# Performance work log

Measured on AMD Instinct MI355X. Metric: run time of the kernel, lower is better.

The kernel has to match this reference:

```python
import jax, jax.numpy as jnp
import numpy as np

EMB = 1024
NH = 16
HD = EMB // NH
FF = 4 * EMB
B, T = 2, 2048
LN_EPS = 1e-5


def setup_inputs() -> dict:
    key = jax.random.key(0)
    ks = jax.random.split(key, 16)
    s = 0.02
    return {
        "x": jax.random.normal(ks[0], (B, T, EMB), jnp.float32),
        "wq": jax.random.normal(ks[1], (EMB, EMB), jnp.float32) * s,
        "bq": jnp.zeros((EMB,), jnp.float32),
        "wk": jax.random.normal(ks[2], (EMB, EMB), jnp.float32) * s,
        "bk": jnp.zeros((EMB,), jnp.float32),
        "wv": jax.random.normal(ks[3], (EMB, EMB), jnp.float32) * s,
        "bv": jnp.zeros((EMB,), jnp.float32),
        "wo": jax.random.normal(ks[4], (EMB, EMB), jnp.float32) * s,
        "bo": jnp.zeros((EMB,), jnp.float32),
        "w1": jax.random.normal(ks[5], (EMB, FF), jnp.float32) * s,
        "b1": jnp.zeros((FF,), jnp.float32),
        "w2": jax.random.normal(ks[6], (FF, EMB), jnp.float32) * s,
        "b2": jnp.zeros((EMB,), jnp.float32),
        "ln1_g": jnp.ones((EMB,), jnp.float32),
        "ln1_b": jnp.zeros((EMB,), jnp.float32),
        "ln2_g": jnp.ones((EMB,), jnp.float32),
        "ln2_b": jnp.zeros((EMB,), jnp.float32),
        "alpha_attn": jnp.float32(0.5),
        "alpha_ff": jnp.float32(0.5),
    }


def _layernorm(x, g, b):
    mu = jnp.mean(x, axis=-1, keepdims=True)
    var = jnp.var(x, axis=-1, keepdims=True)
    return (x - mu) * jax.lax.rsqrt(var + LN_EPS) * g + b


def reference(x, wq, bq, wk, bk, wv, bv, wo, bo, w1, b1, w2, b2,
              ln1_g, ln1_b, ln2_g, ln2_b, alpha_attn, alpha_ff):
    residual = x
    x_ = _layernorm(x, ln1_g, ln1_b)
    # [B,T,E] -> [B,H,T,D]
    def heads(y):
        return y.reshape(B, T, NH, HD).transpose(0, 2, 1, 3)
    q = heads(x_ @ wq + bq)
    k = heads(x_ @ wk + bk)
    v = heads(x_ @ wv + bv)
    scores = jnp.einsum("bhqd,bhkd->bhqk", q, k) / np.sqrt(HD).astype(np.float32)
    causal = jnp.tril(jnp.ones((T, T), dtype=bool))
    scores = jnp.where(causal, scores, -jnp.inf)
    attn = jax.nn.softmax(scores, axis=-1)  # dropout is identity in eval mode
    out = jnp.einsum("bhqk,bhkd->bhqd", attn, v)
    out = out.transpose(0, 2, 1, 3).reshape(B, T, EMB)
    out = out @ wo + bo
    x = residual + alpha_attn * out
    x2 = _layernorm(x, ln2_g, ln2_b)
    ff = jax.nn.gelu(x2 @ w1 + b1, approximate=False) @ w2 + b2
    return x + alpha_ff * ff
```

## Files before the change

### kernel.cpp

```cpp
#include <hip/hip_runtime.h>
#include <cmath>

#define EMB 1024
#define NH 16
#define HD 64
#define FF_DIM 4096
#define BB 2
#define TT 2048
#define NTOK (BB * TT)
#define QKVS 3072
#define SC2F 0.18033688011112042f

typedef _Float16 f16x8 __attribute__((ext_vector_type(8)));
typedef _Float16 f16x4 __attribute__((ext_vector_type(4)));
typedef float f32x4 __attribute__((ext_vector_type(4)));

__device__ __forceinline__ float gelu_fast(float x) {
    float u = x * (1.f + 0.044715f * x * x);
    float e = exp2f(u * 2.302118751f);
    return x - x / (e + 1.f);
}

template <typename TIN>
__global__ __launch_bounds__(256) void ln_kernel(const TIN* __restrict__ xin,
                                                 _Float16* __restrict__ out,
                                                 const float* __restrict__ g,
                                                 const float* __restrict__ bv) {
    int tid = threadIdx.x;
    size_t base = (size_t)blockIdx.x * EMB;
    float v[4];
#pragma unroll
    for (int i = 0; i < 4; ++i) v[i] = (float)xin[base + i * 256 + tid];
    float s = v[0] + v[1] + v[2] + v[3];
    float ss = v[0] * v[0] + v[1] * v[1] + v[2] * v[2] + v[3] * v[3];
#pragma unroll
    for (int off = 32; off > 0; off >>= 1) {
        s += __shfl_down(s, off);
        ss += __shfl_down(ss, off);
    }
    __shared__ float red[8];
    int wave = tid >> 6;
    if ((tid & 63) == 0) { red[wave] = s; red[4 + wave] = ss; }
    __syncthreads();
    s = red[0] + red[1] + red[2] + red[3];
    ss = red[4] + red[5] + red[6] + red[7];
    float mu = s * (1.0f / EMB);
    float var = ss * (1.0f / EMB) - mu * mu;
    float rstd = rsqrtf(var + 1e-5f);
#pragma unroll
    for (int i = 0; i < 4; ++i) {
        int idx = i * 256 + tid;
        float y = (v[i] - mu) * rstd * g[idx] + bv[idx];
        out[base + idx] = (_Float16)y;
    }
}

__global__ __launch_bounds__(256) void prep0_kernel(const float* __restrict__ x,
                                                    _Float16* __restrict__ xn,
                                                    const float* __restrict__ ln1_g,
                                                    const float* __restrict__ ln1_b,
                                                    const float* __restrict__ wq,
                                                    const float* __restrict__ wk,
                                                    const float* __restrict__ wv,
                                                    const float* __restrict__ wo,
                                                    const float* __restrict__ bq,
                                                    const float* __restrict__ bk,
                                                    const float* __restrict__ bv,
                                                    _Float16* __restrict__ wqkvT,
                                                    _Float16* __restrict__ woT,
                                                    float* __restrict__ qkvbias) {
    __shared__ float tile[32][33];
    int blk = blockIdx.x;
    int tid = threadIdx.x;
    if (blk >= 4108) {
        size_t base = (size_t)(blk - 4108) * EMB;
        float v[4];
#pragma unroll
        for (int i = 0; i < 4; ++i) v[i] = x[base + i * 256 + tid];
        float s = v[0] + v[1] + v[2] + v[3];
        float ss = v[0] * v[0] + v[1] * v[1] + v[2] * v[2] + v[3] * v[3];
#pragma unroll
        for (int off = 32; off > 0; off >>= 1) {
            s += __shfl_down(s, off);
            ss += __shfl_down(ss, off);
        }
        float* red = &tile[0][0];
        int wave = tid >> 6;
        if ((tid & 63) == 0) { red[wave] = s; red[4 + wave] = ss; }
        __syncthreads();
        s = red[0] + red[1] + red[2] + red[3];
        ss = red[4] + red[5] + red[6] + red[7];
        float mu = s * (1.0f / EMB);
        float var = ss * (1.0f / EMB) - mu * mu;
        float rstd = rsqrtf(var + 1e-5f);
#pragma unroll
        for (int i = 0; i < 4; ++i) {
            int idx = i * 256 + tid;
            xn[base + idx] = (_Float16)((v[i] - mu) * rstd * ln1_g[idx] + ln1_b[idx]);
        }
        return;
    }
    if (blk >= 4096) {
        int i = (blk - 4096) * 256 + tid;
        qkvbias[i] = i < 1024 ? bq[i] : (i < 2048 ? bk[i - 1024] : bv[i - 2048]);
        return;
    }
    const float* W;
    _Float16* Wt;
    int t = blk & 1023;
    int z = blk >> 10;
    if (z == 0) { W = wq; Wt = wqkvT; }
    else if (z == 1) { W = wk; Wt = wqkvT + 1024 * 1024; }
    else if (z == 2) { W = wv; Wt = wqkvT + 2 * 1024 * 1024; }
    else { W = wo; Wt = woT; }
    int bx = (t & 31) * 32, by = (t >> 5) * 32;
    int tx = tid & 31, ty = tid >> 5;
#pragma unroll
    for (int i = 0; i < 32; i += 8)
        tile[ty + i][tx] = W[(size_t)(by + ty + i) * EMB + bx + tx];
    __syncthreads();
#pragma unroll
    for (int i = 0; i < 32; i += 8)
        Wt[(size_t)(bx + ty + i) * EMB + by + tx] = (_Float16)tile[tx][ty + i];
}

__global__ __launch_bounds__(256) void prep2_kernel(const float* __restrict__ w1,
                                                    const float* __restrict__ w2,
                                                    _Float16* __restrict__ w1T,
                                                    _Float16* __restrict__ w2T) {
    int b = blockIdx.x;
    const float* W;
    _Float16* Wt;
    int K, N, t;
    if (b < 4096) { W = w1; Wt = w1T; K = 1024; N = 4096; t = b; }
    else { W = w2; Wt = w2T; K = 4096; N = 1024; t = b - 4096; }
    int ntx = N >> 5;
    int bx = (t % ntx) * 32, by = (t / ntx) * 32;
    __shared__ float tile[32][33];
    int tx = threadIdx.x & 31, ty = threadIdx.x >> 5;
#pragma unroll
    for (int i = 0; i < 32; i += 8)
        tile[ty + i][tx] = W[(size_t)(by + ty + i) * N + bx + tx];
    __syncthreads();
#pragma unroll
    for (int i = 0; i < 32; i += 8)
        Wt[(size_t)(bx + ty + i) * K + by + tx] = (_Float16)tile[tx][ty + i];
}

__global__ __launch_bounds__(256) void vT_kernel(const _Float16* __restrict__ qkv,
                                                 _Float16* __restrict__ VtG) {
    __shared__ _Float16 tile[64][72];
    int tid = threadIdx.x;
    int bh = blockIdx.y;
    int b = bh >> 4, h = bh & 15;
    int t0 = blockIdx.x * 64;
    const _Float16* src = qkv + (size_t)b * TT * QKVS + 2048 + h * HD;
    int r = tid >> 3;
    int c8 = (tid & 7) * 8;
#pragma unroll
    for (int p = 0; p < 2; ++p)
        *(f16x8*)(&tile[r + p * 32][c8]) =
            *(const f16x8*)(src + (size_t)(t0 + r + p * 32) * QKVS + c8);
    __syncthreads();
#pragma unroll
    for (int p = 0; p < 2; ++p) {
        int d = r + p * 32;
        f16x8 v;
#pragma unroll
        for (int j = 0; j < 8; ++j) v[j] = tile[c8 + j][d];
        *(f16x8*)(VtG + ((size_t)bh * HD + d) * TT + t0 + c8) = v;
    }
}

template <int MODE>
__global__ __launch_bounds__(256) void gemm_f16t(const _Float16* __restrict__ A,
                                                 const _Float16* __restrict__ Bt,
                                                 const float* __restrict__ bias,
                                                 void* __restrict__ outp,
                                                 void* __restrict__ vtg,
                                                 int M, int N, int K, int lda, int ldb) {
    __shared__ _Float16 As[128][64];
    __shared__ _Float16 Bs[128][64];
    int tid = threadIdx.x;
    int lane = tid & 63, w = tid >> 6;
    int quad = lane >> 4, l15 = lane & 15;
    int wm = (w >> 1) * 64, wn = (w & 1) * 64;
    int bM = blockIdx.y * 128, bN = blockIdx.x * 128;
    int lr = lane >> 3;
    int lcs = ((lane & 7) ^ lr) * 8;
    int sw = l15 & 7;
    f32x4 acc[4][4] = {};

    const _Float16* Abase = A + (size_t)(bM + w * 32 + lr) * lda + lcs;
    const _Float16* Bbase = Bt + (size_t)(bN + w * 32 + lr) * ldb + lcs;

    for (int kt = 0; kt < K; kt += 64) {
#pragma unroll
        for (int i = 0; i < 4; ++i) {
            __builtin_amdgcn_global_load_lds(
                (const __attribute__((address_space(1))) void*)(Abase + (size_t)(i * 8) * lda + kt),
                (__attribute__((address_space(3))) void*)(&As[w * 32 + i * 8][0]), 16, 0, 0);
            __builtin_amdgcn_global_load_lds(
                (const __attribute__((address_space(1))) void*)(Bbase + (size_t)(i * 8) * ldb + kt),
                (__attribute__((address_space(3))) void*)(&Bs[w * 32 + i * 8][0]), 16, 0, 0);
        }
        __syncthreads();
#pragma unroll
        for (int ks = 0; ks < 2; ++ks) {
            f16x8 af[4], bf[4];
#pragma unroll
            for (int i = 0; i < 4; ++i) {
                int sc = ((ks * 4 + quad) ^ sw) * 8;
                af[i] = *(const f16x8*)(&As[wm + i * 16 + l15][sc]);
                bf[i] = *(const f16x8*)(&Bs[wn + i * 16 + l15][sc]);
            }
#pragma unroll
            for (int i = 0; i < 4; ++i)
#pragma unroll
                for (int j = 0; j < 4; ++j)
                    acc[i][j] = __builtin_amdgcn_mfma_f32_16x16x32_f16(af[i], bf[j], acc[i][j], 0, 0, 0);
        }
        __syncthreads();
    }

    if (MODE == 6 && vtg != nullptr && bN >= 2048) {
        int bb = bM >> 11;
        int tbase = (bM & 2047) + wm;
#pragma unroll
        for (int i = 0; i < 4; ++i)
#pragma unroll
            for (int j = 0; j < 4; ++j) {
                int hd = bN - 2048 + wn + j * 16;
                int col = 2048 + hd + l15;
                _Float16* dst = (_Float16*)vtg +
                    (((size_t)(bb * 16 + (hd >> 6)) * 64) + (hd & 63) + l15) * TT +
                    tbase + i * 16 + quad * 4;
                f16x4 ov;
#pragma unroll
                for (int r = 0; r < 4; ++r) ov[r] = (_Float16)(acc[i][j][r] + bias[col]);
                *(f16x4*)dst = ov;
            }
        return;
    }

#pragma unroll
    for (int i = 0; i < 4; ++i)
#pragma unroll
        for (int j = 0; j < 4; ++j)
#pragma unroll
            for (int r = 0; r < 4; ++r) {
                int row = bM + wm + i * 16 + quad * 4 + r;
                int col = bN + wn + j * 16 + l15;
                size_t idx = (size_t)row * N + col;
                float vv = acc[i][j][r] + bias[col];
                if (MODE == 6) {
                    if (bN < 1024) vv *= SC2F;
                    ((_Float16*)outp)[idx] = (_Float16)vv;
                } else {
                    ((_Float16*)outp)[idx] = (_Float16)gelu_fast(vv);
                }
            }
}

template <int MODE>
__global__ __launch_bounds__(256) void gemm64(const _Float16* __restrict__ A,
                                              const _Float16* __restrict__ Bt,
                                              const float* __restrict__ bias,
                                              void* __restrict__ outp,
                                              const void* __restrict__ residp,
                                              const float* __restrict__ alphap,
                                              int M, int N, int K, int lda, int ldb) {
    __shared__ _Float16 As[128][64];
    __shared__ _Float16 Bs[64][64];
    int tid = threadIdx.x;
    int lane = tid & 63, w = tid >> 6;
    int quad = lane >> 4, l15 = lane & 15;
    int wm = w * 32;
    int bM = blockIdx.y * 128, bN = blockIdx.x * 64;
    int lr = lane >> 3;
    int lcs = ((lane & 7) ^ lr) * 8;
    int sw = l15 & 7;
    int kz = (MODE == 7) ? blockIdx.z * K : 0;
    f32x4 acc[2][4] = {};

    const _Float16* Abase = A + (size_t)(bM + w * 32 + lr) * lda + kz + lcs;
    const _Float16* Bbase = Bt + (size_t)(bN + w * 16 + lr) * ldb + kz + lcs;

    for (int kt = 0; kt < K; kt += 64) {
#pragma unroll
        for (int i = 0; i < 4; ++i)
            __builtin_amdgcn_global_load_lds(
                (const __attribute__((address_space(1))) void*)(Abase + (size_t)(i * 8) * lda + kt),
                (__attribute__((address_space(3))) void*)(&As[w * 32 + i * 8][0]), 16, 0, 0);
#pragma unroll
        for (int i = 0; i < 2; ++i)
            __builtin_amdgcn_global_load_lds(
                (const __attribute__((address_space(1))) void*)(Bbase + (size_t)(i * 8) * ldb + kt),
                (__attribute__((address_space(3))) void*)(&Bs[w * 16 + i * 8][0]), 16, 0, 0);
        __syncthreads();
#pragma unroll
        for (int ks = 0; ks < 2; ++ks) {
            int sc = ((ks * 4 + quad) ^ sw) * 8;
            f16x8 af[2], bf[4];
#pragma unroll
            for (int i = 0; i < 2; ++i)
                af[i] = *(const f16x8*)(&As[wm + i * 16 + l15][sc]);
#pragma unroll
            for (int j = 0; j < 4; ++j)
                bf[j] = *(const f16x8*)(&Bs[j * 16 + l15][sc]);
#pragma unroll
            for (int i = 0; i < 2; ++i)
#pragma unroll
                for (int j = 0; j < 4; ++j)
                    acc[i][j] = __builtin_amdgcn_mfma_f32_16x16x32_f16(af[i], bf[j], acc[i][j], 0, 0, 0);
        }
        __syncthreads();
    }

    float alpha = 0.f;
    if (MODE == 2 || MODE == 5) alpha = alphap[0];
    _Float16* pout = nullptr;
    if (MODE == 7) pout = blockIdx.z ? (_Float16*)(void*)residp : (_Float16*)outp;
#pragma unroll
    for (int i = 0; i < 2; ++i)
#pragma unroll
        for (int j = 0; j < 4; ++j)
#pragma unroll
            for (int r = 0; r < 4; ++r) {
                int row = bM + wm + i * 16 + quad * 4 + r;
                int col = bN + j * 16 + l15;
                size_t idx = (size_t)row * N + col;
                if (MODE == 7) {
                    pout[idx] = (_Float16)acc[i][j][r];
                } else if (MODE == 4) {
                    ((float*)outp)[idx] = acc[i][j][r];
                } else if (MODE == 2) {
                    float vv = acc[i][j][r] + bias[col];
                    float rsd = ((const float*)residp)[idx];
                    ((_Float16*)outp)[idx] = (_Float16)(rsd + alpha * vv);
                } else {
                    float vv = acc[i][j][r] + bias[col];
                    float prev = ((float*)outp)[idx];
                    float rsd = (float)((const _Float16*)residp)[idx];
                    ((float*)outp)[idx] = rsd + alpha * (prev + vv);
                }
            }
}

__global__ __launch_bounds__(256) void ff2_reduce_kernel(const _Float16* __restrict__ p0,
                                                         const _Float16* __restrict__ p1,
                                                         const _Float16* __restrict__ xmid,
                                                         const float* __restrict__ b2,
                                                         const float* __restrict__ alphap,
                                                         float* __restrict__ out) {
    int i = (blockIdx.x * 256 + threadIdx.x) * 8;
    float alpha = alphap[0];
    f16x8 a = *(const f16x8*)(p0 + i);
    f16x8 b = *(const f16x8*)(p1 + i);
    f16x8 xm = *(const f16x8*)(xmid + i);
    int col = i & 1023;
#pragma unroll
    for (int k = 0; k < 8; ++k)
        out[i + k] = (float)xm[k] + alpha * ((float)a[k] + (float)b[k] + b2[col + k]);
}

#define QT 64
#define KT2 64
#define NEG_BIG (-1e30f)
__global__ __launch_bounds__(256) void attn_mfma_kernel(const _Float16* __restrict__ qkv,
                                                        const _Float16* __restrict__ VtG,
                                                        _Float16* __restrict__ O) {
    __shared__ _Float16 Ks[64][72];
    __shared__ _Float16 Vt[64][72];
    __shared__ _Float16 Ps[4][16][68];
    int tid = threadIdx.x;
    int lane = tid & 63, w = tid >> 6;
    int quad = lane >> 4, l15 = lane & 15;
    int bh = blockIdx.x;
    int b = bh >> 4, h = bh & 15;
    int y = blockIdx.y;
    int qt = (y & 1) ? (31 - (y >> 1)) : (y >> 1);
    int q0 = qt * QT;
    const _Float16* Qh = qkv + (size_t)b * TT * QKVS + h * HD;
    const _Float16* Kh = Qh + 1024;
    const _Float16* Vrows = VtG + (size_t)bh * HD * TT;

    int m0 = q0 + w * 16;
    f16x8 aq0 = *(const f16x8*)(Qh + (size_t)(m0 + l15) * QKVS + quad * 8);
    f16x8 aq1 = *(const f16x8*)(Qh + (size_t)(m0 + l15) * QKVS + 32 + quad * 8);

    f32x4 Oacc[4] = {};
    float lrow[4] = {0.f, 0.f, 0.f, 0.f};

    int rr = tid >> 3;
    int c8 = (tid & 7) * 8;
    const _Float16* Kp0 = Kh + (size_t)rr * QKVS + c8;
    const _Float16* Kp1 = Kh + (size_t)(rr + 32) * QKVS + c8;
    const _Float16* Vp0 = Vrows + (size_t)rr * TT + c8;
    const _Float16* Vp1 = Vrows + (size_t)(rr + 32) * TT + c8;

    f16x8 kreg0 = *(const f16x8*)(Kp0);
    f16x8 kreg1 = *(const f16x8*)(Kp1);
    f16x8 vreg0 = *(const f16x8*)(Vp0);
    f16x8 vreg1 = *(const f16x8*)(Vp1);

    int nt = qt + 1;
    for (int t = 0; t < nt; ++t) {
        int t0 = t * KT2;
        __syncthreads();
        *(f16x8*)(&Ks[rr][c8]) = kreg0;
        *(f16x8*)(&Ks[rr + 32][c8]) = kreg1;
        *(f16x8*)(&Vt[rr][c8]) = vreg0;
        *(f16x8*)(&Vt[rr + 32][c8]) = vreg1;
        __syncthreads();
        if (t + 1 < nt) {
            size_t koff = (size_t)(t0 + KT2) * QKVS;
            kreg0 = *(const f16x8*)(Kp0 + koff);
            kreg1 = *(const f16x8*)(Kp1 + koff);
            vreg0 = *(const f16x8*)(Vp0 + t0 + KT2);
            vreg1 = *(const f16x8*)(Vp1 + t0 + KT2);
        }

        f32x4 Sacc[4] = {};
#pragma unroll
        for (int nc = 0; nc < 4; ++nc) {
            f16x8 bk0 = *(const f16x8*)(&Ks[nc * 16 + l15][quad * 8]);
            f16x8 bk1 = *(const f16x8*)(&Ks[nc * 16 + l15][32 + quad * 8]);
            Sacc[nc] = __builtin_amdgcn_mfma_f32_16x16x32_f16(aq0, bk0, Sacc[nc], 0, 0, 0);
            Sacc[nc] = __builtin_amdgcn_mfma_f32_16x16x32_f16(aq1, bk1, Sacc[nc], 0, 0, 0);
        }

        if (t0 == q0) {
#pragma unroll
            for (int nc = 0; nc < 4; ++nc) {
                int key = t0 + nc * 16 + l15;
#pragma unroll
                for (int i = 0; i < 4; ++i)
                    if (key > m0 + quad * 4 + i) Sacc[nc][i] = NEG_BIG;
            }
        }

#pragma unroll
        for (int nc = 0; nc < 4; ++nc)
#pragma unroll
            for (int i = 0; i < 4; ++i) {
                float p = exp2f(Sacc[nc][i]);
                lrow[i] += p;
                Ps[w][quad * 4 + i][nc * 16 + l15] = (_Float16)p;
            }
        __asm__ __volatile__("s_waitcnt lgkmcnt(0)" ::: "memory");

        f16x8 ap0 = *(const f16x8*)(&Ps[w][l15][quad * 8]);
        f16x8 ap1 = *(const f16x8*)(&Ps[w][l15][32 + quad * 8]);
#pragma unroll
        for (int nc = 0; nc < 4; ++nc) {
            int d = nc * 16 + l15;
            f16x8 bv0 = *(const f16x8*)(&Vt[d][quad * 8]);
            f16x8 bv1 = *(const f16x8*)(&Vt[d][32 + quad * 8]);
            Oacc[nc] = __builtin_amdgcn_mfma_f32_16x16x32_f16(ap0, bv0, Oacc[nc], 0, 0, 0);
            Oacc[nc] = __builtin_amdgcn_mfma_f32_16x16x32_f16(ap1, bv1, Oacc[nc], 0, 0, 0);
        }
    }

#pragma unroll
    for (int off = 1; off < 16; off <<= 1)
#pragma unroll
        for (int i = 0; i < 4; ++i) lrow[i] += __shfl_xor(lrow[i], off);
#pragma unroll
    for (int i = 0; i < 4; ++i) lrow[i] = 1.0f / lrow[i];
    _Float16* Oh = O + (size_t)b * TT * EMB + h * HD;
#pragma unroll
    for (int nc = 0; nc < 4; ++nc)
#pragma unroll
        for (int i = 0; i < 4; ++i) {
            int row = m0 + quad * 4 + i;
            Oh[(size_t)row * EMB + nc * 16 + l15] = (_Float16)(Oacc[nc][i] * lrow[i]);
        }
}

extern "C" void kernel_launch(void* const* d_in, const int* in_sizes, int n_in,
                              void* d_out, int out_size, void* d_ws, size_t ws_size,
                              hipStream_t stream) {
    const float* x = (const float*)d_in[0];
    const float* wq = (const float*)d_in[1];
    const float* bq = (const float*)d_in[2];
    const float* wk = (const float*)d_in[3];
    const float* bk = (const float*)d_in[4];
    const float* wv = (const float*)d_in[5];
    const float* bv = (const float*)d_in[6];
    const float* wo = (const float*)d_in[7];
    const float* bo = (const float*)d_in[8];
    const float* w1 = (const float*)d_in[9];
    const float* b1 = (const float*)d_in[10];
    const float* w2 = (const float*)d_in[11];
    const float* b2 = (const float*)d_in[12];
    const float* ln1_g = (const float*)d_in[13];
    const float* ln1_b = (const float*)d_in[14];
    const float* ln2_g = (const float*)d_in[15];
    const float* ln2_b = (const float*)d_in[16];
    const float* alpha_attn = (const float*)d_in[17];
    const float* alpha_ff = (const float*)d_in[18];

    const size_t SL = (size_t)8 * 1024 * 1024;
    char* ws = (char*)d_ws;
    _Float16* xn = (_Float16*)(ws);
    _Float16* qkv = (_Float16*)(ws + SL);
    _Float16* wqkvT = (_Float16*)(ws + 4 * SL);
    float* qkvbias = (float*)(ws + 4 * SL + 6 * 1024 * 1024);
    _Float16* attnout = (_Float16*)(ws);
    _Float16* xmid = (_Float16*)(ws + SL);
    _Float16* x2 = (_Float16*)(ws + 2 * SL);
    _Float16* w1T = (_Float16*)(ws);
    _Float16* w2T = (_Float16*)(ws + 3 * SL);
    _Float16* ff1 = (_Float16*)(ws + 4 * SL);
    bool bigws = ws_size >= (size_t)64 * 1024 * 1024;
    _Float16* VtG = bigws ? (_Float16*)(ws + 5 * SL) : (_Float16*)(ws + 4 * SL);
    _Float16* woT = bigws ? (_Float16*)(ws + 6 * SL) : (_Float16*)(ws + 5 * SL);
    _Float16* part0 = (_Float16*)(ws);
    _Float16* part1 = (_Float16*)(ws + 2 * SL);

    prep0_kernel<<<8204, 256, 0, stream>>>(x, xn, ln1_g, ln1_b, wq, wk, wv, wo,
                                           bq, bk, bv, wqkvT, woT, qkvbias);

    gemm_f16t<6><<<dim3(QKVS / 128, NTOK / 128), 256, 0, stream>>>(
        xn, wqkvT, qkvbias, qkv, bigws ? (void*)VtG : nullptr, NTOK, QKVS, EMB, EMB, EMB);
    if (!bigws)
        vT_kernel<<<dim3(TT / 64, BB * NH), 256, 0, stream>>>(qkv, VtG);

    attn_mfma_kernel<<<dim3(BB * NH, TT / QT), 256, 0, stream>>>(qkv, VtG, attnout);

    gemm64<2><<<dim3(EMB / 64, NTOK / 128), 256, 0, stream>>>(
        attnout, woT, bo, xmid, x, alpha_attn, NTOK, EMB, EMB, EMB, EMB);

    ln_kernel<_Float16><<<NTOK, 256, 0, stream>>>(xmid, x2, ln2_g, ln2_b);

    prep2_kernel<<<8192, 256, 0, stream>>>(w1, w2, w1T, w2T);

    if (bigws) {
        gemm_f16t<1><<<dim3(FF_DIM / 128, NTOK / 128), 256, 0, stream>>>(
            x2, w1T, b1, ff1, nullptr, NTOK, FF_DIM, EMB, EMB, EMB);
        gemm64<7><<<dim3(EMB / 64, NTOK / 128, 2), 256, 0, stream>>>(
            ff1, w2T, nullptr, part0, part1, nullptr, NTOK, EMB, 2048, FF_DIM, FF_DIM);
        ff2_reduce_kernel<<<NTOK * EMB / 8 / 256, 256, 0, stream>>>(
            part0, part1, xmid, b2, alpha_ff, (float*)d_out);
    } else {
        const int NC = 2048;
        for (int hh = 0; hh < 2; ++hh) {
            const _Float16* w1Th = w1T + (size_t)hh * NC * EMB;
            const _Float16* w2Th = w2T + (size_t)hh * NC;
            gemm_f16t<1><<<dim3(NC / 128, NTOK / 128), 256, 0, stream>>>(
                x2, w1Th, b1 + hh * NC, ff1, nullptr, NTOK, NC, EMB, EMB, EMB);
            if (hh == 0)
                gemm64<4><<<dim3(EMB / 64, NTOK / 128), 256, 0, stream>>>(
                    ff1, w2Th, nullptr, d_out, nullptr, nullptr, NTOK, EMB, NC, NC, FF_DIM);
            else
                gemm64<5><<<dim3(EMB / 64, NTOK / 128), 256, 0, stream>>>(
                    ff1, w2Th, b2, d_out, xmid, alpha_ff, NTOK, EMB, NC, NC, FF_DIM);
        }
    }
}
```

Before: 369.4 us.

## Pair complementary causal query tiles per block to share K/V tile loads

```diff
diff --git a/kernel.cpp b/kernel.cpp
--- a/kernel.cpp
+++ b/kernel.cpp
@@ -365,27 +365,29 @@
 }
 
 #define QT 64
-#define KT2 64
 #define NEG_BIG (-1e30f)
-__global__ __launch_bounds__(256) void attn_mfma_kernel(const _Float16* __restrict__ qkv,
+__global__ __launch_bounds__(512) void attn_mfma_kernel(const _Float16* __restrict__ qkv,
                                                         const _Float16* __restrict__ VtG,
                                                         _Float16* __restrict__ O) {
     __shared__ _Float16 Ks[64][72];
     __shared__ _Float16 Vt[64][72];
-    __shared__ _Float16 Ps[4][16][68];
+    __shared__ _Float16 Ps[8][16][68];
     int tid = threadIdx.x;
     int lane = tid & 63, w = tid >> 6;
     int quad = lane >> 4, l15 = lane & 15;
     int bh = blockIdx.x;
     int b = bh >> 4, h = bh & 15;
     int y = blockIdx.y;
-    int qt = (y & 1) ? (31 - (y >> 1)) : (y >> 1);
+    int seg = w >> 2, ws = w & 3;
+    int qt = seg ? y : (31 - y);
     int q0 = qt * QT;
+    int ntw = qt + 1;
+    int ntmax = 32 - y;
     const _Float16* Qh = qkv + (size_t)b * TT * QKVS + h * HD;
     const _Float16* Kh = Qh + 1024;
     const _Float16* Vrows = VtG + (size_t)bh * HD * TT;
 
-    int m0 = q0 + w * 16;
+    int m0 = q0 + ws * 16;
     f16x8 aq0 = *(const f16x8*)(Qh + (size_t)(m0 + l15) * QKVS + quad * 8);
     f16x8 aq1 = *(const f16x8*)(Qh + (size_t)(m0 + l15) * QKVS + 32 + quad * 8);
 
@@ -394,34 +396,26 @@
 
     int rr = tid >> 3;
     int c8 = (tid & 7) * 8;
-    const _Float16* Kp0 = Kh + (size_t)rr * QKVS + c8;
-    const _Float16* Kp1 = Kh + (size_t)(rr + 32) * QKVS + c8;
-    const _Float16* Vp0 = Vrows + (size_t)rr * TT + c8;
-    const _Float16* Vp1 = Vrows + (size_t)(rr + 32) * TT + c8;
-
-    f16x8 kreg0 = *(const f16x8*)(Kp0);
-    f16x8 kreg1 = *(const f16x8*)(Kp1);
-    f16x8 vreg0 = *(const f16x8*)(Vp0);
-    f16x8 vreg1 = *(const f16x8*)(Vp1);
-
-    int nt = qt + 1;
-    for (int t = 0; t < nt; ++t) {
-        int t0 = t * KT2;
-        __syncthreads();
-        *(f16x8*)(&Ks[rr][c8]) = kreg0;
-        *(f16x8*)(&Ks[rr + 32][c8]) = kreg1;
-        *(f16x8*)(&Vt[rr][c8]) = vreg0;
-        *(f16x8*)(&Vt[rr + 32][c8]) = vreg1;
-        __syncthreads();
-        if (t + 1 < nt) {
-            size_t koff = (size_t)(t0 + KT2) * QKVS;
-            kreg0 = *(const f16x8*)(Kp0 + koff);
-            kreg1 = *(const f16x8*)(Kp1 + koff);
-            vreg0 = *(const f16x8*)(Vp0 + t0 + KT2);
-            vreg1 = *(const f16x8*)(Vp1 + t0 + KT2);
-        }
+    const _Float16* Kp = Kh + (size_t)rr * QKVS + c8;
+    const _Float16* Vp = Vrows + (size_t)rr * TT + c8;
+
+    f16x8 kreg = *(const f16x8*)(Kp);
+    f16x8 vreg = *(const f16x8*)(Vp);
+
+    for (int t = 0; t < ntmax; ++t) {
+        int t0 = t * 64;
+        __syncthreads();
+        *(f16x8*)(&Ks[rr][c8]) = kreg;
+        *(f16x8*)(&Vt[rr][c8]) = vreg;
+        __syncthreads();
+        if (t + 1 < ntmax) {
+            kreg = *(const f16x8*)(Kp + (size_t)(t0 + 64) * QKVS);
+            vreg = *(const f16x8*)(Vp + t0 + 64);
+        }
+        if (t >= ntw) continue;
 
         f32x4 Sacc[4] = {};
+        __builtin_amdgcn_s_setprio(1);
 #pragma unroll
         for (int nc = 0; nc < 4; ++nc) {
             f16x8 bk0 = *(const f16x8*)(&Ks[nc * 16 + l15][quad * 8]);
@@ -429,6 +423,7 @@
             Sacc[nc] = __builtin_amdgcn_mfma_f32_16x16x32_f16(aq0, bk0, Sacc[nc], 0, 0, 0);
             Sacc[nc] = __builtin_amdgcn_mfma_f32_16x16x32_f16(aq1, bk1, Sacc[nc], 0, 0, 0);
         }
+        __builtin_amdgcn_s_setprio(0);
 
         if (t0 == q0) {
 #pragma unroll
@@ -452,6 +447,7 @@
 
         f16x8 ap0 = *(const f16x8*)(&Ps[w][l15][quad * 8]);
         f16x8 ap1 = *(const f16x8*)(&Ps[w][l15][32 + quad * 8]);
+        __builtin_amdgcn_s_setprio(1);
 #pragma unroll
         for (int nc = 0; nc < 4; ++nc) {
             int d = nc * 16 + l15;
@@ -460,6 +456,7 @@
             Oacc[nc] = __builtin_amdgcn_mfma_f32_16x16x32_f16(ap0, bv0, Oacc[nc], 0, 0, 0);
             Oacc[nc] = __builtin_amdgcn_mfma_f32_16x16x32_f16(ap1, bv1, Oacc[nc], 0, 0, 0);
         }
+        __builtin_amdgcn_s_setprio(0);
     }
 
 #pragma unroll
@@ -527,7 +524,7 @@
     if (!bigws)
         vT_kernel<<<dim3(TT / 64, BB * NH), 256, 0, stream>>>(qkv, VtG);
 
-    attn_mfma_kernel<<<dim3(BB * NH, TT / QT), 256, 0, stream>>>(qkv, VtG, attnout);
+    attn_mfma_kernel<<<dim3(BB * NH, TT / QT / 2), 512, 0, stream>>>(qkv, VtG, attnout);
 
     gemm64<2><<<dim3(EMB / 64, NTOK / 128), 256, 0, stream>>>(
         attnout, woT, bo, xmid, x, alpha_attn, NTOK, EMB, EMB, EMB, EMB);
```

After: 375.8 us. Within noise of the previous version (+1.7%).
